# Kernel optimization log

Measured on AMD Instinct MI355X. Metric: run time of the kernel, lower is better.

Reference implementation:

```python
import jax, jax.numpy as jnp
import numpy as np

E, C_IN, NUM_CLASSES = 4, 3, 100
HW = 32
C1, C2, GC = 64, 128, 16
FC_IN = C2 * (HW // 4) * (HW // 4)  # 128*8*8 = 8192


def _conv(x, w, b):
    # x: [B,Cin,H,W], w: [Cout,Cin,3,3] -> [B,Cout,H,W] (SAME padding)
    y = jax.lax.conv_general_dilated(x, w, (1, 1), 'SAME',
                                     dimension_numbers=('NCHW', 'OIHW', 'NCHW'))
    return y + b[None, :, None, None]


def _maxpool2(x):
    return jax.lax.reduce_window(x, -jnp.inf, jax.lax.max,
                                 (1, 1, 2, 2), (1, 1, 2, 2), 'VALID')


def setup_inputs() -> dict:
    key = jax.random.key(0)
    ks = jax.random.split(key, 12)
    s = lambda k, shape, fan: (jax.random.normal(k, shape, jnp.float32) / np.sqrt(fan))
    return {
        'x': jax.random.normal(ks[0], (1024, C_IN, HW, HW), jnp.float32),
        # gating network
        'gate_cw': s(ks[1], (GC, C_IN, 3, 3), C_IN * 9),
        'gate_cb': jnp.zeros((GC,), jnp.float32),
        'gate_fw': s(ks[2], (E, GC), GC),
        'gate_fb': jnp.zeros((E,), jnp.float32),
        # stacked expert params [E, ...]
        'e_c1w': s(ks[3], (E, C1, C_IN, 3, 3), C_IN * 9),
        'e_c1b': jnp.zeros((E, C1), jnp.float32),
        'e_c2w': s(ks[4], (E, C2, C1, 3, 3), C1 * 9),
        'e_c2b': jnp.zeros((E, C2), jnp.float32),
        'e_fw': s(ks[5], (E, NUM_CLASSES, FC_IN), FC_IN),
        'e_fb': jnp.zeros((E, NUM_CLASSES), jnp.float32),
    }


def reference(x, gate_cw, gate_cb, gate_fw, gate_fb,
              e_c1w, e_c1b, e_c2w, e_c2b, e_fw, e_fb):
    B = x.shape[0]
    # --- gating: conv -> relu -> global avg pool -> linear -> softmax ---
    g = jax.nn.relu(_conv(x, gate_cw, gate_cb))            # [B,GC,H,W]
    g = g.mean(axis=(2, 3))                                # [B,GC]
    router_probs = jax.nn.softmax(g @ gate_fw.T + gate_fb) # [B,E]

    best_weights = router_probs.max(axis=1)                # [B]
    best_indices = jnp.argmax(router_probs, axis=1)        # [B]

    # --- hard top-1 dispatch: mask-and-combine (same math as gather/scatter) ---
    final_output = jnp.zeros((B, NUM_CLASSES), x.dtype)
    for e in range(E):  # fixed small expert count, structurally distinct params
        h = jax.nn.relu(_conv(x, e_c1w[e], e_c1b[e]))      # [B,64,32,32]
        h = _maxpool2(h)                                   # [B,64,16,16]
        h = jax.nn.relu(_conv(h, e_c2w[e], e_c2b[e]))      # [B,128,16,16]
        h = _maxpool2(h)                                   # [B,128,8,8]
        logits = h.reshape(B, -1) @ e_fw[e].T + e_fb[e]    # [B,100]
        mask = (best_indices == e)[:, None]
        final_output = final_output + jnp.where(
            mask, logits * best_weights[:, None], 0.0)

    mean_probs = router_probs.mean(axis=0)
    aux_loss = jnp.mean((mean_probs - 1.0 / E) ** 2)
    return final_output, router_probs, aux_loss
```

## Files before the change

### kernel.cpp

```cpp
#include <hip/hip_runtime.h>
#include <hip/hip_bf16.h>
#include <cstdint>


#define B_TOT 1024

typedef __attribute__((ext_vector_type(8))) short short8;
typedef __attribute__((ext_vector_type(16))) float f32x16;

__device__ __forceinline__ ushort f2bf(float f) {
  uint32_t u = __float_as_uint(f);
  u += 0x7fffu + ((u >> 16) & 1u);
  return (ushort)(u >> 16);
}

__global__ __launch_bounds__(256) void k_prep(
    const float* __restrict__ x, const float* __restrict__ gcw,
    const float* __restrict__ gcb, const float* __restrict__ gfw,
    const float* __restrict__ gfb, float* __restrict__ probs,
    float* __restrict__ best_w, int* __restrict__ best_idx,
    const float* __restrict__ w2, ushort* __restrict__ wp,
    const float* __restrict__ w1, ushort* __restrict__ wA,
    const float* __restrict__ efw, ushort* __restrict__ wfc) {
  __shared__ float xs[3 * 34 * 34];
  __shared__ float red[4 * 16];
  __shared__ float gm[16];
  __shared__ float lgs[4];
  const int blk = blockIdx.x;
  const int t = threadIdx.x;

  if (blk < 1024) {
    const int b = blk;
    const float* xb = x + (size_t)b * 3072;

    for (int c = t; c < 3468; c += 256) {
      const int ci = c / 1156;
      const int rem = c - ci * 1156;
      const int y = rem / 34;
      const int xx = rem - y * 34;
      const int gy = y - 1, gx = xx - 1;
      float v = 0.f;
      if (gy >= 0 && gy < 32 && gx >= 0 && gx < 32) v = xb[ci * 1024 + gy * 32 + gx];
      xs[c] = v;
    }
    __syncthreads();

    const int r = t >> 3;
    const int c0 = (t & 7) * 4;

    float accp[16][4];
#pragma unroll
    for (int c = 0; c < 16; c++)
#pragma unroll
      for (int p = 0; p < 4; p++) accp[c][p] = 0.f;

#pragma unroll
    for (int ci = 0; ci < 3; ci++) {
      float pv[3][6];
#pragma unroll
      for (int dy = 0; dy < 3; dy++) {
        const float* row = xs + ci * 1156 + (r + dy) * 34 + c0;
#pragma unroll
        for (int dx = 0; dx < 6; dx++) pv[dy][dx] = row[dx];
      }
#pragma unroll
      for (int c = 0; c < 16; c++) {
        const float* wr = gcw + (c * 3 + ci) * 9;
#pragma unroll
        for (int ky = 0; ky < 3; ky++)
#pragma unroll
          for (int kx = 0; kx < 3; kx++) {
            const float wv = wr[ky * 3 + kx];
#pragma unroll
            for (int p = 0; p < 4; p++)
              accp[c][p] += wv * pv[ky][kx + p];
          }
      }
    }

    float sums[16];
#pragma unroll
    for (int c = 0; c < 16; c++) {
      const float bb = gcb[c];
      float s = 0.f;
#pragma unroll
      for (int p = 0; p < 4; p++) s += fmaxf(accp[c][p] + bb, 0.f);
      sums[c] = s;
    }

    const int wave = t >> 6, lane = t & 63;
#pragma unroll
    for (int c = 0; c < 16; c++) {
      float v = sums[c];
      for (int o = 32; o > 0; o >>= 1) v += __shfl_down(v, o);
      if (lane == 0) red[wave * 16 + c] = v;
    }
    __syncthreads();
    if (t < 16)
      gm[t] = (red[t] + red[16 + t] + red[32 + t] + red[48 + t]) * (1.f / 1024.f);
    __syncthreads();
    if (t < 4) {
      float sum = gfb[t];
#pragma unroll
      for (int c = 0; c < 16; c++) sum += gm[c] * gfw[t * 16 + c];
      lgs[t] = sum;
    }
    __syncthreads();
    if (t == 0) {
      const float m = fmaxf(fmaxf(lgs[0], lgs[1]), fmaxf(lgs[2], lgs[3]));
      float ex[4], ssum = 0.f;
#pragma unroll
      for (int e = 0; e < 4; e++) { ex[e] = __expf(lgs[e] - m); ssum += ex[e]; }
      const float inv = 1.f / ssum;
      int bi = 0; float bp = ex[0];
#pragma unroll
      for (int e = 1; e < 4; e++) if (ex[e] > bp) { bp = ex[e]; bi = e; }
#pragma unroll
      for (int e = 0; e < 4; e++) probs[b * 4 + e] = ex[e] * inv;
      best_w[b] = bp * inv;
      best_idx[b] = bi;
    }
  } else if (blk < 2176) {
    const int i = (blk - 1024) * 256 + t;
    const int j = i & 7;
    const int cout = (i >> 3) & 127;
    const int kb = (i >> 10) & 7;
    const int kkE = i >> 13;
    const int kk = kkE - (kkE / 9) * 9;
    const int e = kkE / 9;
    const int ci = kb * 8 + j;
    const float f = w2[(size_t)(((e * 128 + cout) * 64 + ci) * 9) + kk];
    wp[i] = f2bf(f);
  } else if (blk < 2304) {
    const int i = (blk - 2176) * 256 + t;
    const int j = i & 7;
    const int cout = (i >> 3) & 63;
    const int kb = (i >> 9) & 3;
    const int e = i >> 11;
    const int k = kb * 8 + j;
    float f = 0.f;
    if (k < 27) {
      const int ci = k / 9;
      const int kk = k - ci * 9;
      f = w1[(size_t)(((e * 64 + cout) * 3 + ci) * 9) + kk];
    }
    wA[i] = f2bf(f);
  } else {
    const int i = (blk - 2304) * 256 + t;
    const int j = i & 7;
    const int cout = (i >> 3) & 127;
    const int kb = (i >> 10) & 1023;
    const int e = i >> 20;
    const int k = kb * 8 + j;
    float f = 0.f;
    if (cout < 100) f = efw[((size_t)(e * 100 + cout)) * 8192 + k];
    wfc[i] = f2bf(f);
  }
}

__global__ __launch_bounds__(256) void k_route(
    const float* __restrict__ probs, const int* __restrict__ best_idx_g,
    int* __restrict__ off_g, int* __restrict__ counts_g,
    int* __restrict__ order, float* __restrict__ aux_out) {
  __shared__ int cnt[4], ofs[5], cl[4];
  __shared__ short bidx[1024];
  __shared__ float red[16];
  const int t = threadIdx.x;
  if (t < 4) { cnt[t] = 0; cl[t] = 0; }
  __syncthreads();

  float asum[4] = {0.f, 0.f, 0.f, 0.f};
  for (int s = t; s < B_TOT; s += 256) {
    const int bi = best_idx_g[s];
    bidx[s] = (short)bi;
    atomicAdd(&cnt[bi], 1);
#pragma unroll
    for (int e = 0; e < 4; e++) asum[e] += probs[s * 4 + e];
  }
  __syncthreads();

  if (t == 0) {
    int o = 0;
#pragma unroll
    for (int e = 0; e < 4; e++) { ofs[e] = o; o += ((cnt[e] + 31) & ~31); }
    ofs[4] = o;
#pragma unroll
    for (int i = 0; i < 5; i++) off_g[i] = ofs[i];
#pragma unroll
    for (int e = 0; e < 4; e++) counts_g[e] = cnt[e];
  }
  __syncthreads();

  for (int s = t; s < B_TOT; s += 256) {
    const int e2 = bidx[s];
    const int slot = ofs[e2] + atomicAdd(&cl[e2], 1);
    order[slot] = s;
  }

  const int wave = t >> 6, lane = t & 63;
#pragma unroll
  for (int e = 0; e < 4; e++) {
    float v = asum[e];
    for (int o = 32; o > 0; o >>= 1) v += __shfl_down(v, o);
    if (lane == 0) red[wave * 4 + e] = v;
  }
  __syncthreads();
  if (t == 0) {
    float aux = 0.f;
#pragma unroll
    for (int e = 0; e < 4; e++) {
      const float mp = (red[e] + red[4 + e] + red[8 + e] + red[12 + e]) * (1.f / 1024.f);
      const float d = mp - 0.25f;
      aux += d * d;
    }
    aux_out[0] = aux * 0.25f;
  }
}

__global__ __launch_bounds__(256) void k_conv1(
    const float* __restrict__ x, const ushort* __restrict__ wA,
    const float* __restrict__ b1, const int* __restrict__ best_idx,
    ushort* __restrict__ h1q) {
  __shared__ ushort xs[1020];
  __shared__ __align__(16) ushort Bl[256 * 32];
  const int blk = blockIdx.x;
  const int b = blk >> 2;
  const int q = blk & 3;
  const int t = threadIdx.x;
  const int e = __builtin_amdgcn_readfirstlane(best_idx[b]);
  const float* xb = x + (size_t)b * 3072;
  const float* b1e = b1 + (size_t)e * 64;

  for (int c = t; c < 1020; c += 256) {
    const int ci = c / 340;
    const int rem = c - ci * 340;
    const int hr = rem / 34;
    const int hc = rem - hr * 34;
    const int gr = 8 * q + hr - 1, gc = hc - 1;
    float v = 0.f;
    if (gr >= 0 && gr < 32 && gc >= 0 && gc < 32) v = xb[ci * 1024 + gr * 32 + gc];
    xs[c] = f2bf(v);
  }
  __syncthreads();

  {
    const int rr = t >> 5, cc = t & 31;
    ushort us[32];
#pragma unroll
    for (int k = 0; k < 32; k++) {
      ushort v = 0;
      if (k < 27) {
        const int ci = k / 9;
        const int tap = k - ci * 9;
        const int dy = tap / 3, dx = tap - dy * 3;
        v = xs[ci * 340 + (rr + dy) * 34 + cc + dx];
      }
      us[k] = v;
    }
    uint4 pk[2];
    uint* pu = (uint*)pk;
#pragma unroll
    for (int w = 0; w < 8; w++)
      pu[w] = (uint)us[w * 2] | ((uint)us[w * 2 + 1] << 16);
    *(uint4*)(Bl + t * 32) = pk[0];
    *(uint4*)(Bl + t * 32 + 8) = pk[1];
    uint4 pk2[2];
    uint* pu2 = (uint*)pk2;
#pragma unroll
    for (int w = 0; w < 8; w++)
      pu2[w] = (uint)us[16 + w * 2] | ((uint)us[16 + w * 2 + 1] << 16);
    *(uint4*)(Bl + t * 32 + 16) = pk2[0];
    *(uint4*)(Bl + t * 32 + 24) = pk2[1];
  }
  __syncthreads();

  const int lane = t & 63;
  const int wv = t >> 6;
  const int g = wv & 1;
  const int nh = wv >> 1;
  const int ln = lane & 31;
  const int half = lane >> 5;

  const short8 af0 = *(const short8*)(wA + (size_t)(((e * 4 + half) * 64) + g * 32 + ln) * 8);
  const short8 af1 = *(const short8*)(wA + (size_t)(((e * 4 + 2 + half) * 64) + g * 32 + ln) * 8);

  f32x16 acc[4];
#pragma unroll
  for (int tt = 0; tt < 4; tt++)
#pragma unroll
    for (int i = 0; i < 16; i++) acc[tt][i] = 0.f;

#pragma unroll
  for (int tt = 0; tt < 4; tt++) {
    const ushort* bcol = Bl + (size_t)((nh * 4 + tt) * 32 + ln) * 32;
    const short8 b0 = *(const short8*)(bcol + half * 8);
    const short8 b1v = *(const short8*)(bcol + 16 + half * 8);
    acc[tt] = __builtin_amdgcn_mfma_f32_32x32x16_bf16(af0, b0, acc[tt], 0, 0, 0);
    acc[tt] = __builtin_amdgcn_mfma_f32_32x32x16_bf16(af1, b1v, acc[tt], 0, 0, 0);
  }

  float bias[16];
#pragma unroll
  for (int r = 0; r < 16; r++)
    bias[r] = b1e[g * 32 + (r & 3) + 8 * (r >> 2) + 4 * half];

  const int pc = ln >> 1;
#pragma unroll
  for (int j = 0; j < 2; j++) {
    float pw[16];
#pragma unroll
    for (int r = 0; r < 16; r++) {
      float v = fmaxf(acc[2 * j][r], acc[2 * j + 1][r]);
      v = fmaxf(v, __shfl_xor(v, 1));
      pw[r] = fmaxf(v + bias[r], 0.f);
    }
    if ((lane & 1) == 0) {
      const int pos = (4 * q + nh * 2 + j) * 16 + pc;
      ushort* dst = h1q + (size_t)b * 16384 + pos * 8 + 4 * half;
#pragma unroll
      for (int rg = 0; rg < 4; rg++) {
        uint2 pk;
        pk.x = (uint)f2bf(pw[rg * 4 + 0]) | ((uint)f2bf(pw[rg * 4 + 1]) << 16);
        pk.y = (uint)f2bf(pw[rg * 4 + 2]) | ((uint)f2bf(pw[rg * 4 + 3]) << 16);
        *(uint2*)(dst + (g * 4 + rg) * 2048) = pk;
      }
    }
  }
}

__global__ __launch_bounds__(512, 2) void k_conv2(
    const ushort* __restrict__ h1q, const ushort* __restrict__ wp,
    const float* __restrict__ b2, const int* __restrict__ best_idx,
    ushort* __restrict__ h2q) {
  __shared__ uint4 st[1440];
  const int blk = blockIdx.x;
  const int b = blk >> 1;
  const int q = blk & 1;
  const int t = threadIdx.x;
  const int e = __builtin_amdgcn_readfirstlane(best_idx[b]);
  const ushort* wpe = wp + (size_t)e * 73728;

  for (int c = t; c < 1440; c += 512) {
    const int row = c / 144;
    const int rem = c - row * 144;
    const int cig = rem / 18;
    const int col = rem - cig * 18;
    const int gy = 8 * q - 1 + row, gx = col - 1;
    uint4 v = make_uint4(0u, 0u, 0u, 0u);
    if (gy >= 0 && gy < 16 && gx >= 0 && gx < 16)
      v = *(const uint4*)(h1q + (size_t)b * 16384 + cig * 2048 + (gy * 16 + gx) * 8);
    st[c] = v;
  }
  __syncthreads();

  const int lane = t & 63;
  const int wv = t >> 6;
  const int g = wv & 1;
  const int h = wv >> 1;
  const int half = lane >> 5;
  const int n = lane & 31;
  const int drow = n >> 4;
  const int col15 = n & 15;
  const int cm0 = g * 64;

  const short* sbs = (const short*)st;
  const ushort* abase = wpe + (size_t)(half * 128 + cm0 + n) * 8;

  f32x16 acc[2];
#pragma unroll
  for (int m = 0; m < 2; m++)
#pragma unroll
    for (int i = 0; i < 16; i++) acc[m][i] = 0.f;

  short8 a0[4], a1[4];
#pragma unroll
  for (int c4 = 0; c4 < 4; c4++) {
    a0[c4] = *(const short8*)(abase + c4 * 2048);
    a1[c4] = *(const short8*)(abase + c4 * 2048 + 256);
  }

#pragma unroll
  for (int kk = 0; kk < 9; kk++) {
    const int ky = kk / 3;
    const int kx = kk - ky * 3;
#pragma unroll
    for (int c4 = 0; c4 < 4; c4++) {
      const int kb = c4 * 2 + half;
      const int rin = 2 * h + drow + ky;
      const int cin = col15 + kx;
      const short8 bf = *(const short8*)(sbs + ((rin * 8 + kb) * 18 + cin) * 8);
      acc[0] = __builtin_amdgcn_mfma_f32_32x32x16_bf16(a0[c4], bf, acc[0], 0, 0, 0);
      acc[1] = __builtin_amdgcn_mfma_f32_32x32x16_bf16(a1[c4], bf, acc[1], 0, 0, 0);
      if (kk < 8) {
        a0[c4] = *(const short8*)(abase + (kk + 1) * 8192 + c4 * 2048);
        a1[c4] = *(const short8*)(abase + (kk + 1) * 8192 + c4 * 2048 + 256);
      }
    }
  }
  __syncthreads();

  ushort* pls = (ushort*)st;
#pragma unroll
  for (int m = 0; m < 2; m++) {
#pragma unroll
    for (int r = 0; r < 16; r++) {
      float v = acc[m][r];
      v = fmaxf(v, __shfl_xor(v, 1));
      v = fmaxf(v, __shfl_xor(v, 16));
      if ((lane & 17) == 0) {
        const int rowm = (r & 3) + 8 * (r >> 2) + 4 * half;
        const int cout = cm0 + m * 32 + rowm;
        const int prl = h;
        const int pc = (n >> 1) & 7;
        pls[cout * 32 + prl * 8 + pc] = f2bf(fmaxf(v + b2[e * 128 + cout], 0.f));
      }
    }
  }
  __syncthreads();

  {
    const int f16 = t;
    const int flat = f16 * 8;
    const int cout = flat >> 5;
    const int pos32 = flat & 31;
    uint4* dst = (uint4*)(h2q + (size_t)b * 8192 + cout * 64 + 32 * q + pos32);
    *dst = ((const uint4*)pls)[f16];
  }
}

__global__ __launch_bounds__(256) void k_fc(
    const ushort* __restrict__ h2q, const ushort* __restrict__ wfc,
    const int* __restrict__ order, const int* __restrict__ off,
    const int* __restrict__ counts, float* __restrict__ partial) {
  __shared__ ushort bs[32 * 32 * 8];
  __shared__ int sid[32];
  const int tix = blockIdx.x;
  const int ks = blockIdx.y;
  const int base = tix * 32;
  if (base >= off[4]) return;
  int e = 0;
#pragma unroll
  for (int i = 1; i < 4; i++) if (base >= off[i]) e = i;
  const int vend = off[e] + counts[e];
  const int t = threadIdx.x;
  if (t < 32) {
    const int pos = base + t;
    sid[t] = (pos < vend) ? order[pos] : -1;
  }
  __syncthreads();

  const int lane = t & 63;
  const int wv = t >> 6;
  const int half = lane >> 5;
  const int mn = lane & 31;
  const int cout0 = wv * 32;
  const int ss = t & 31;
  const int kgrp = t >> 5;
  const int srow = sid[ss] >= 0 ? sid[ss] : 0;
  const ushort* arow = h2q + (size_t)srow * 8192;

  f32x16 acc;
#pragma unroll
  for (int i = 0; i < 16; i++) acc[i] = 0.f;

  const ushort* wbase = wfc + ((size_t)e * 1024 + (size_t)ks * 64) * 1024;
  const short* sb = (const short*)bs;

#pragma unroll
  for (int ch = 0; ch < 2; ch++) {
    const int k0g = ks * 512 + ch * 256;
    if (ch) __syncthreads();
#pragma unroll
    for (int p = 0; p < 4; p++) {
      const int kb = p * 8 + kgrp;
      const uint4 v = *(const uint4*)(arow + k0g + kb * 8);
      *(uint4*)(bs + (kb * 32 + ss) * 8) = v;
    }
    __syncthreads();
#pragma unroll
    for (int kk = 0; kk < 16; kk++) {
      const int kbl = kk * 2 + half;
      const short8 af = *(const short8*)(wbase +
          ((size_t)(ch * 32 + kbl) * 128 + cout0 + mn) * 8);
      const short8 bf = *(const short8*)(sb + (kbl * 32 + mn) * 8);
      acc = __builtin_amdgcn_mfma_f32_32x32x16_bf16(af, bf, acc, 0, 0, 0);
    }
  }

  float* pks = partial + (size_t)ks * 147456;
#pragma unroll
  for (int r = 0; r < 16; r++) {
    const int cout = cout0 + (r & 3) + 8 * (r >> 2) + 4 * half;
    pks[(size_t)cout * 1152 + base + mn] = acc[r];
  }
}

__global__ __launch_bounds__(256) void k_red(
    const float* __restrict__ partial, const float* __restrict__ efb,
    const int* __restrict__ order, const int* __restrict__ off,
    const int* __restrict__ counts, const float* __restrict__ best_w,
    float* __restrict__ out) {
  const int slot = blockIdx.x * 256 + threadIdx.x;
  if (slot >= off[4]) return;
  int e = 0;
#pragma unroll
  for (int i = 1; i < 4; i++) if (slot >= off[i]) e = i;
  if (slot - off[e] >= counts[e]) return;
  const int s = order[slot];
  const float bw = best_w[s];
  const int o0 = blockIdx.y * 4;
#pragma unroll
  for (int j = 0; j < 4; j++) {
    const int o = o0 + j;
    float sum = 0.f;
#pragma unroll
    for (int ks = 0; ks < 16; ks++)
      sum += partial[(size_t)ks * 147456 + (size_t)o * 1152 + slot];
    out[(size_t)s * 100 + o] = (sum + efb[e * 100 + o]) * bw;
  }
}

extern "C" void kernel_launch(void* const* d_in, const int* in_sizes, int n_in,
                              void* d_out, int out_size, void* d_ws, size_t ws_size,
                              hipStream_t stream) {
  const float* x   = (const float*)d_in[0];
  const float* gcw = (const float*)d_in[1];
  const float* gcb = (const float*)d_in[2];
  const float* gfw = (const float*)d_in[3];
  const float* gfb = (const float*)d_in[4];
  const float* c1w = (const float*)d_in[5];
  const float* c1b = (const float*)d_in[6];
  const float* c2w = (const float*)d_in[7];
  const float* c2b = (const float*)d_in[8];
  const float* efw = (const float*)d_in[9];
  const float* efb = (const float*)d_in[10];
  float* out = (float*)d_out;
  float* ws  = (float*)d_ws;

  float*  best_w   = ws + 16384;
  int*    best_idx = (int*)(ws + 17408);
  int*    counts   = (int*)(ws + 18432);
  int*    off      = (int*)(ws + 18440);
  int*    order    = (int*)(ws + 18448);
  ushort* wp       = (ushort*)(ws + 20480);
  ushort* wfc      = (ushort*)(ws + 167936);
  ushort* h1       = (ushort*)(ws + 2265088);
  ushort* h2q      = (ushort*)(ws + 10653696);
  float*  partial  = ws + 14848000;
  ushort* wA       = (ushort*)(ws + 17207296);

  float* probs = out + 102400;
  float* aux   = out + 106496;

  k_prep<<<18688, 256, 0, stream>>>(x, gcw, gcb, gfw, gfb, probs, best_w,
                                    best_idx, c2w, wp, c1w, wA, efw, wfc);
  k_route<<<1, 256, 0, stream>>>(probs, best_idx, off, counts, order, aux);
  k_conv1<<<4096, 256, 0, stream>>>(x, wA, c1b, best_idx, h1);
  k_conv2<<<2048, 512, 0, stream>>>(h1, wp, c2b, best_idx, h2q);
  dim3 g5(36, 16);
  k_fc<<<g5, 256, 0, stream>>>(h2q, wfc, order, off, counts, partial);
  dim3 g6(5, 25);
  k_red<<<g6, 256, 0, stream>>>(partial, efb, order, off, counts, best_w, out);
}
```

Baseline: 214.7 us.

## Fold routing into prep via last-block counter and fuse FC split-K reduction with atomics

The single-block routing kernel is removed. Its work now runs in the last gating block of k_prep, chosen with an atomic ticket counter and thread fences. The separate split-K reduction kernel and its partial buffer are also removed: k_fc scales its accumulators by the routing weight, adds the bias on the first K-split, and atomically adds into a zeroed output. This saves two kernel launches and a partial-buffer round trip. The cost is two memsets, float atomics with nondeterministic summation order, and a serialized tail block inside k_prep.

```diff
diff --git a/kernel.cpp b/kernel.cpp
--- a/kernel.cpp
+++ b/kernel.cpp
@@ -19,6 +19,9 @@
     const float* __restrict__ gcb, const float* __restrict__ gfw,
     const float* __restrict__ gfb, float* __restrict__ probs,
     float* __restrict__ best_w, int* __restrict__ best_idx,
+    int* __restrict__ ctr, int* __restrict__ off_g,
+    int* __restrict__ counts_g, int* __restrict__ order,
+    float* __restrict__ aux_out,
     const float* __restrict__ w2, ushort* __restrict__ wp,
     const float* __restrict__ w1, ushort* __restrict__ wA,
     const float* __restrict__ efw, ushort* __restrict__ wfc) {
@@ -26,6 +29,9 @@
   __shared__ float red[4 * 16];
   __shared__ float gm[16];
   __shared__ float lgs[4];
+  __shared__ int tk;
+  __shared__ int cnt[4], ofs[5], cl[4];
+  __shared__ short bidx[1024];
   const int blk = blockIdx.x;
   const int t = threadIdx.x;
 
@@ -119,6 +125,58 @@
       for (int e = 0; e < 4; e++) probs[b * 4 + e] = ex[e] * inv;
       best_w[b] = bp * inv;
       best_idx[b] = bi;
+    }
+
+    __threadfence();
+    if (t == 0) tk = atomicAdd(ctr, 1);
+    __syncthreads();
+    if (tk == 1023) {
+      __threadfence();
+      if (t < 4) { cnt[t] = 0; cl[t] = 0; }
+      __syncthreads();
+      float asum[4] = {0.f, 0.f, 0.f, 0.f};
+      for (int s = t; s < B_TOT; s += 256) {
+        const int bi = best_idx[s];
+        bidx[s] = (short)bi;
+        atomicAdd(&cnt[bi], 1);
+#pragma unroll
+        for (int e2 = 0; e2 < 4; e2++) asum[e2] += probs[s * 4 + e2];
+      }
+      __syncthreads();
+      if (t == 0) {
+        int o = 0;
+#pragma unroll
+        for (int e2 = 0; e2 < 4; e2++) { ofs[e2] = o; o += ((cnt[e2] + 31) & ~31); }
+        ofs[4] = o;
+#pragma unroll
+        for (int i = 0; i < 5; i++) off_g[i] = ofs[i];
+#pragma unroll
+        for (int e2 = 0; e2 < 4; e2++) counts_g[e2] = cnt[e2];
+      }
+      __syncthreads();
+      for (int s = t; s < B_TOT; s += 256) {
+        const int e2 = bidx[s];
+        const int slot = ofs[e2] + atomicAdd(&cl[e2], 1);
+        order[slot] = s;
+      }
+      const int wave2 = t >> 6, lane2 = t & 63;
+#pragma unroll
+      for (int e2 = 0; e2 < 4; e2++) {
+        float v = asum[e2];
+        for (int o = 32; o > 0; o >>= 1) v += __shfl_down(v, o);
+        if (lane2 == 0) red[wave2 * 4 + e2] = v;
+      }
+      __syncthreads();
+      if (t == 0) {
+        float aux = 0.f;
+#pragma unroll
+        for (int e2 = 0; e2 < 4; e2++) {
+          const float mp = (red[e2] + red[4 + e2] + red[8 + e2] + red[12 + e2]) * (1.f / 1024.f);
+          const float d = mp - 0.25f;
+          aux += d * d;
+        }
+        aux_out[0] = aux * 0.25f;
+      }
     }
   } else if (blk < 2176) {
     const int i = (blk - 1024) * 256 + t;
@@ -158,65 +216,6 @@
   }
 }
 
-__global__ __launch_bounds__(256) void k_route(
-    const float* __restrict__ probs, const int* __restrict__ best_idx_g,
-    int* __restrict__ off_g, int* __restrict__ counts_g,
-    int* __restrict__ order, float* __restrict__ aux_out) {
-  __shared__ int cnt[4], ofs[5], cl[4];
-  __shared__ short bidx[1024];
-  __shared__ float red[16];
-  const int t = threadIdx.x;
-  if (t < 4) { cnt[t] = 0; cl[t] = 0; }
-  __syncthreads();
-
-  float asum[4] = {0.f, 0.f, 0.f, 0.f};
-  for (int s = t; s < B_TOT; s += 256) {
-    const int bi = best_idx_g[s];
-    bidx[s] = (short)bi;
-    atomicAdd(&cnt[bi], 1);
-#pragma unroll
-    for (int e = 0; e < 4; e++) asum[e] += probs[s * 4 + e];
-  }
-  __syncthreads();
-
-  if (t == 0) {
-    int o = 0;
-#pragma unroll
-    for (int e = 0; e < 4; e++) { ofs[e] = o; o += ((cnt[e] + 31) & ~31); }
-    ofs[4] = o;
-#pragma unroll
-    for (int i = 0; i < 5; i++) off_g[i] = ofs[i];
-#pragma unroll
-    for (int e = 0; e < 4; e++) counts_g[e] = cnt[e];
-  }
-  __syncthreads();
-
-  for (int s = t; s < B_TOT; s += 256) {
-    const int e2 = bidx[s];
-    const int slot = ofs[e2] + atomicAdd(&cl[e2], 1);
-    order[slot] = s;
-  }
-
-  const int wave = t >> 6, lane = t & 63;
-#pragma unroll
-  for (int e = 0; e < 4; e++) {
-    float v = asum[e];
-    for (int o = 32; o > 0; o >>= 1) v += __shfl_down(v, o);
-    if (lane == 0) red[wave * 4 + e] = v;
-  }
-  __syncthreads();
-  if (t == 0) {
-    float aux = 0.f;
-#pragma unroll
-    for (int e = 0; e < 4; e++) {
-      const float mp = (red[e] + red[4 + e] + red[8 + e] + red[12 + e]) * (1.f / 1024.f);
-      const float d = mp - 0.25f;
-      aux += d * d;
-    }
-    aux_out[0] = aux * 0.25f;
-  }
-}
-
 __global__ __launch_bounds__(256) void k_conv1(
     const float* __restrict__ x, const ushort* __restrict__ wA,
     const float* __restrict__ b1, const int* __restrict__ best_idx,
@@ -431,7 +430,8 @@
 __global__ __launch_bounds__(256) void k_fc(
     const ushort* __restrict__ h2q, const ushort* __restrict__ wfc,
     const int* __restrict__ order, const int* __restrict__ off,
-    const int* __restrict__ counts, float* __restrict__ partial) {
+    const int* __restrict__ counts, const float* __restrict__ best_w,
+    const float* __restrict__ efb, float* __restrict__ out) {
   __shared__ ushort bs[32 * 32 * 8];
   __shared__ int sid[32];
   const int tix = blockIdx.x;
@@ -487,36 +487,19 @@
     }
   }
 
-  float* pks = partial + (size_t)ks * 147456;
-#pragma unroll
-  for (int r = 0; r < 16; r++) {
-    const int cout = cout0 + (r & 3) + 8 * (r >> 2) + 4 * half;
-    pks[(size_t)cout * 1152 + base + mn] = acc[r];
-  }
-}
-
-__global__ __launch_bounds__(256) void k_red(
-    const float* __restrict__ partial, const float* __restrict__ efb,
-    const int* __restrict__ order, const int* __restrict__ off,
-    const int* __restrict__ counts, const float* __restrict__ best_w,
-    float* __restrict__ out) {
-  const int slot = blockIdx.x * 256 + threadIdx.x;
-  if (slot >= off[4]) return;
-  int e = 0;
-#pragma unroll
-  for (int i = 1; i < 4; i++) if (slot >= off[i]) e = i;
-  if (slot - off[e] >= counts[e]) return;
-  const int s = order[slot];
-  const float bw = best_w[s];
-  const int o0 = blockIdx.y * 4;
-#pragma unroll
-  for (int j = 0; j < 4; j++) {
-    const int o = o0 + j;
-    float sum = 0.f;
-#pragma unroll
-    for (int ks = 0; ks < 16; ks++)
-      sum += partial[(size_t)ks * 147456 + (size_t)o * 1152 + slot];
-    out[(size_t)s * 100 + o] = (sum + efb[e * 100 + o]) * bw;
+  const int scol = sid[mn];
+  if (scol >= 0) {
+    const float bw = best_w[scol];
+    float* orow = out + (size_t)scol * 100;
+#pragma unroll
+    for (int r = 0; r < 16; r++) {
+      const int cout = cout0 + (r & 3) + 8 * (r >> 2) + 4 * half;
+      if (cout < 100) {
+        float v = acc[r] * bw;
+        if (ks == 0) v += efb[e * 100 + cout] * bw;
+        atomicAdd(&orow[cout], v);
+      }
+    }
   }
 }
 
@@ -542,23 +525,23 @@
   int*    counts   = (int*)(ws + 18432);
   int*    off      = (int*)(ws + 18440);
   int*    order    = (int*)(ws + 18448);
+  int*    ctr      = (int*)(ws + 19600);
   ushort* wp       = (ushort*)(ws + 20480);
   ushort* wfc      = (ushort*)(ws + 167936);
   ushort* h1       = (ushort*)(ws + 2265088);
   ushort* h2q      = (ushort*)(ws + 10653696);
-  float*  partial  = ws + 14848000;
   ushort* wA       = (ushort*)(ws + 17207296);
 
   float* probs = out + 102400;
   float* aux   = out + 106496;
 
+  hipMemsetAsync(ctr, 0, sizeof(int), stream);
+  hipMemsetAsync(out, 0, 102400 * sizeof(float), stream);
   k_prep<<<18688, 256, 0, stream>>>(x, gcw, gcb, gfw, gfb, probs, best_w,
-                                    best_idx, c2w, wp, c1w, wA, efw, wfc);
-  k_route<<<1, 256, 0, stream>>>(probs, best_idx, off, counts, order, aux);
+                                    best_idx, ctr, off, counts, order, aux,
+                                    c2w, wp, c1w, wA, efw, wfc);
   k_conv1<<<4096, 256, 0, stream>>>(x, wA, c1b, best_idx, h1);
   k_conv2<<<2048, 512, 0, stream>>>(h1, wp, c2b, best_idx, h2q);
   dim3 g5(36, 16);
-  k_fc<<<g5, 256, 0, stream>>>(h2q, wfc, order, off, counts, partial);
-  dim3 g6(5, 25);
-  k_red<<<g6, 256, 0, stream>>>(partial, efb, order, off, counts, best_w, out);
+  k_fc<<<g5, 256, 0, stream>>>(h2q, wfc, order, off, counts, best_w, efb, out);
 }
```

Result: slower. 353.0 us (+64.4%).
